# Performance work log

Measured on AMD Instinct MI355X. Metric: run time of the kernel, lower is better.

Reference implementation:

```python
import jax, jax.numpy as jnp
import numpy as np

B, H, W = 8, 160, 160
L = H * W  # 25600, matches nn.LayerNorm(25600)
QDIM = KDIM = MID = OUT = 256
HEADS = 8
HEAD_DIM = MID // HEADS  # 32
LN_EPS = 1e-5


def conv1x1(x, w, b):
    # x: [N,C,H,W], w: [O,C], b: [O] -> [N,O,H,W]
    return jnp.einsum('nchw,oc->nohw', x, w) + b[None, :, None, None]


def setup_inputs() -> dict:
    key = jax.random.key(0)
    ks = jax.random.split(key, 12)
    s = 0.02
    return {
        'query': jax.random.normal(ks[0], (B, QDIM, H, W), jnp.float32),
        'key': jax.random.normal(ks[1], (B, KDIM, H, W), jnp.float32),
        'Wq': jax.random.normal(ks[2], (MID, QDIM), jnp.float32) * s,
        'bq': jnp.zeros((MID,), jnp.float32),
        'Wk': jax.random.normal(ks[3], (MID, KDIM), jnp.float32) * s,
        'bk': jnp.zeros((MID,), jnp.float32),
        'Wv': jax.random.normal(ks[4], (MID, KDIM), jnp.float32) * s,
        'bv': jnp.zeros((MID,), jnp.float32),
        'Wo': jax.random.normal(ks[5], (OUT, MID), jnp.float32) * s,
        'bo': jnp.zeros((OUT,), jnp.float32),
        'gamma': jnp.ones((L,), jnp.float32),
        'beta': jnp.zeros((L,), jnp.float32),
    }


def reference(query, key, Wq, bq, Wk, bk, Wv, bv, Wo, bo, gamma, beta):
    # 1x1-conv projections, flatten spatial dims to L
    q = conv1x1(query, Wq, bq).reshape(B, HEADS, HEAD_DIM, L)
    k = conv1x1(key, Wk, bk).reshape(B, HEADS, HEAD_DIM, L)
    v = conv1x1(key, Wv, bv).reshape(B, HEADS, HEAD_DIM, L)
    # NOTE: faithful to the source, scores contract over L (spatial), giving
    # a [B, heads, head_dim, head_dim] channel-attention matrix.
    scores = jnp.einsum('nhdl,nhel->nhde', q, k) / (KDIM ** 0.5)
    attn = jax.nn.softmax(scores, axis=-1)  # dropout is identity at eval
    out = jnp.einsum('nhde,nhel->nhdl', attn, v).reshape(B, MID, L)
    # LayerNorm over the flattened spatial axis (size 25600)
    mu = jnp.mean(out, axis=-1, keepdims=True)
    var = jnp.var(out, axis=-1, keepdims=True)
    out = (out - mu) * jax.lax.rsqrt(var + LN_EPS) * gamma + beta
    out = out.reshape(B, MID, H, W)
    return conv1x1(out, Wo, bo)
```

## Files before the change

kernel.cpp:

```cpp
#include <hip/hip_runtime.h>
#include <hip/hip_bf16.h>
#include <stdint.h>

#define LROW 25600
#define NCH 256
#define LN_EPS 1e-5f

typedef float f32x4 __attribute__((ext_vector_type(4)));
typedef __bf16 bf16x8 __attribute__((ext_vector_type(8)));

__device__ __forceinline__ bf16x8 cvt8(f32x4 a, f32x4 b) {
  bf16x8 r;
  r[0] = (__bf16)a[0]; r[1] = (__bf16)a[1]; r[2] = (__bf16)a[2]; r[3] = (__bf16)a[3];
  r[4] = (__bf16)b[0]; r[5] = (__bf16)b[1]; r[6] = (__bf16)b[2]; r[7] = (__bf16)b[3];
  return r;
}

__device__ __forceinline__ void wg_bar() {
  asm volatile("s_waitcnt lgkmcnt(0)\n\ts_barrier" ::: "memory");
}

__global__ __launch_bounds__(1024, 4) void gram_k(
    const float* __restrict__ qg, const float* __restrict__ kg,
    float* __restrict__ Gd, float* __restrict__ Gkkd,
    float* __restrict__ sq, float* __restrict__ sk) {
  __shared__ __align__(16) __bf16 lA[256 * 32];
  __shared__ __align__(16) __bf16 lB[256 * 32];

  const int bid = blockIdx.x;
  const int x = bid & 7;
  int n = bid >> 3;
  int b = 0, s = 0;
  for (int bb = 0; bb < 8; ++bb) {
    const int gsl = (x - bb) & 7;
    const int gs = (21 * gsl + 7) >> 3, ge = (21 * gsl + 28) >> 3;
    const int ks = (11 * gsl + 7) >> 3, ke = (11 * gsl + 18) >> 3;
    const int cnt = (ge - gs) + (ke - ks);
    if (n < cnt) {
      b = bb;
      s = (n < ge - gs) ? (gs + n) : (21 + ks + (n - (ge - gs)));
      break;
    }
    n -= cnt;
  }

  const int mat = (s < 21) ? 0 : 1;
  const int idx = mat ? (s - 21) : s;
  const int parts = mat ? 11 : 21;
  const int c0 = (800 * idx) / parts, c1 = (800 * (idx + 1)) / parts;
  const int nc = c1 - c0;
  const int tid = threadIdx.x;
  const int w = tid >> 6, lane = tid & 63;
  const int wr = w >> 2, wc = w & 3;
  const int lr = lane & 15, g = lane >> 4;
  const float* Ag = (mat ? kg : qg) + (size_t)b * NCH * LROW;
  const float* Bg = kg + (size_t)b * NCH * LROW;

  const int rowS = tid >> 2, uS = tid & 3;
  const int uSw = uS ^ ((rowS >> 1) & 3);
  const size_t gOff = (size_t)rowS * LROW + uS * 8;
  __bf16* ldsA_dst = lA + rowS * 32 + uSw * 8;
  __bf16* ldsB_dst = lB + rowS * 32 + uSw * 8;

  const f32x4 zero = {0.f, 0.f, 0.f, 0.f};
  f32x4 acc[4][4];
#pragma unroll
  for (int i = 0; i < 4; ++i)
#pragma unroll
    for (int j = 0; j < 4; ++j) acc[i][j] = zero;

  float rsum = 0.f;

  auto LOADG = [&](int c, f32x4* d) {
    const float* pa = Ag + gOff + (size_t)c * 32;
    d[0] = *(const f32x4*)pa;
    d[1] = *(const f32x4*)(pa + 4);
    if (mat == 0) {
      const float* pb = Bg + gOff + (size_t)c * 32;
      d[2] = *(const f32x4*)pb;
      d[3] = *(const f32x4*)(pb + 4);
    }
  };

  auto PROCESS = [&](f32x4* d) {
#pragma unroll
    for (int e = 0; e < 4; ++e) rsum += d[0][e] + d[1][e];
    *(bf16x8*)ldsA_dst = cvt8(d[0], d[1]);
    if (mat == 0) *(bf16x8*)ldsB_dst = cvt8(d[2], d[3]);
    wg_bar();
    const __bf16* Bp = mat ? lA : lB;
    bf16x8 af[4];
#pragma unroll
    for (int i = 0; i < 4; ++i) {
      const int row = wr * 64 + i * 16 + lr;
      const int u = g ^ ((row >> 1) & 3);
      af[i] = *(const bf16x8*)(lA + row * 32 + u * 8);
    }
#pragma unroll
    for (int j = 0; j < 4; ++j) {
      const int row = wc * 64 + j * 16 + lr;
      const int u = g ^ ((row >> 1) & 3);
      bf16x8 bfj = *(const bf16x8*)(Bp + row * 32 + u * 8);
#pragma unroll
      for (int i = 0; i < 4; ++i)
        acc[i][j] = __builtin_amdgcn_mfma_f32_16x16x32_bf16(af[i], bfj, acc[i][j], 0, 0, 0);
    }
    wg_bar();
  };

  f32x4 bA[4], bB[4];
  LOADG(c0, bA);
  int cc = 0;
  for (; cc + 2 <= nc; cc += 2) {
    LOADG(c0 + cc + 1, bB);
    PROCESS(bA);
    if (cc + 2 < nc) LOADG(c0 + cc + 2, bA);
    PROCESS(bB);
  }
  if (cc < nc) PROCESS(bA);

  atomicAdd((mat ? sk : sq) + b * NCH + rowS, rsum);

  float* Gout = (mat ? Gkkd : Gd) + (size_t)b * 65536;
#pragma unroll
  for (int i = 0; i < 4; ++i)
#pragma unroll
    for (int j = 0; j < 4; ++j) {
      const int col = wc * 64 + j * 16 + lr;
      const int row0 = wr * 64 + i * 16 + g * 4;
#pragma unroll
      for (int r = 0; r < 4; ++r)
        atomicAdd(&Gout[(size_t)(row0 + r) * NCH + col], acc[i][j][r]);
    }
}

__global__ __launch_bounds__(256) void attn_k(
    const float* __restrict__ G, const float* __restrict__ sq,
    const float* __restrict__ sk,
    const float* __restrict__ Wq, const float* __restrict__ bq,
    const float* __restrict__ Wk, const float* __restrict__ bk,
    const float* __restrict__ Wv, const float* __restrict__ bv,
    float* __restrict__ M, float* __restrict__ cvec) {
  __shared__ float Wql[32][257];
  __shared__ float Wkl[32][257];
  __shared__ float QGl[32][257];
  __shared__ float Sl[32][33];
  __shared__ float Al[32][33];
  __shared__ float ul[32], wl[32];
  const int b = blockIdx.x >> 3, h = blockIdx.x & 7;
  const int t = threadIdx.x;
  const float* Gb = G + (size_t)b * 65536;

  for (int i = 0; i < 32; ++i) {
    int idx = i * 256 + t;
    int d = idx >> 8, c = idx & 255;
    Wql[d][c] = Wq[(h * 32 + d) * 256 + c];
    Wkl[d][c] = Wk[(h * 32 + d) * 256 + c];
  }
  __syncthreads();
  {
    float a[32];
#pragma unroll
    for (int d = 0; d < 32; ++d) a[d] = 0.f;
    for (int c = 0; c < 256; ++c) {
      float gv = Gb[c * 256 + t];
#pragma unroll
      for (int d = 0; d < 32; ++d) a[d] += Wql[d][c] * gv;
    }
    for (int d = 0; d < 32; ++d) QGl[d][t] = a[d];
  }
  if (t < 32) {
    float u = 0.f, wv = 0.f;
    for (int c = 0; c < 256; ++c) {
      u += Wql[t][c] * sq[b * 256 + c];
      wv += Wkl[t][c] * sk[b * 256 + c];
    }
    ul[t] = u; wl[t] = wv;
  }
  __syncthreads();
  for (int i = 0; i < 4; ++i) {
    int idx = i * 256 + t;
    int d = idx >> 5, e = idx & 31;
    float sv = 0.f;
    for (int c = 0; c < 256; ++c) sv += QGl[d][c] * Wkl[e][c];
    float bqd = bq[h * 32 + d], bke = bk[h * 32 + e];
    Sl[d][e] = (sv + ul[d] * bke + bqd * wl[e] + 25600.f * bqd * bke) * (1.f / 16.f);
  }
  __syncthreads();
  if (t < 32) {
    float m = -1e30f;
    for (int e = 0; e < 32; ++e) m = fmaxf(m, Sl[t][e]);
    float ssum = 0.f;
    for (int e = 0; e < 32; ++e) { float p = __expf(Sl[t][e] - m); Al[t][e] = p; ssum += p; }
    float is = 1.f / ssum;
    for (int e = 0; e < 32; ++e) Al[t][e] *= is;
  }
  __syncthreads();
  {
    float a[32];
#pragma unroll
    for (int d = 0; d < 32; ++d) a[d] = 0.f;
    for (int e = 0; e < 32; ++e) {
      float wv = Wv[(h * 32 + e) * 256 + t];
#pragma unroll
      for (int d = 0; d < 32; ++d) a[d] += Al[d][e] * wv;
    }
    for (int d = 0; d < 32; ++d) M[((size_t)b * 256 + h * 32 + d) * 256 + t] = a[d];
  }
  if (t < 32) {
    float cv = 0.f;
    for (int e = 0; e < 32; ++e) cv += Al[t][e] * bv[h * 32 + e];
    cvec[b * 256 + h * 32 + t] = cv;
  }
}

__global__ __launch_bounds__(256) void stats_k(
    const float* __restrict__ Gkk, const float* __restrict__ M,
    const float* __restrict__ sk, const float* __restrict__ cvec,
    float* __restrict__ mu, float* __restrict__ inv) {
  __shared__ float Ml[32][257];
  __shared__ float Ql[32][257];
  const int b = blockIdx.x >> 3, cb = blockIdx.x & 7;
  const int t = threadIdx.x;
  const float* Gk = Gkk + (size_t)b * 65536;
  for (int i = 0; i < 32; ++i) {
    int idx = i * 256 + t;
    Ml[idx >> 8][idx & 255] = M[((size_t)b * 256 + cb * 32 + (idx >> 8)) * 256 + (idx & 255)];
  }
  __syncthreads();
  {
    float a[32];
#pragma unroll
    for (int c = 0; c < 32; ++c) a[c] = 0.f;
    for (int cc = 0; cc < 256; ++cc) {
      float gv = Gk[cc * 256 + t];
#pragma unroll
      for (int c = 0; c < 32; ++c) a[c] += Ml[c][cc] * gv;
    }
    for (int c = 0; c < 32; ++c) Ql[c][t] = a[c];
  }
  __syncthreads();
  if (t < 32) {
    float qf = 0.f, msk = 0.f;
    for (int j = 0; j < 256; ++j) {
      qf += Ql[t][j] * Ml[t][j];
      msk += Ml[t][j] * sk[b * 256 + j];
    }
    int c = cb * 32 + t;
    float cv = cvec[b * 256 + c];
    float muv = msk * (1.f / 25600.f) + cv;
    float sum2 = qf + 2.f * cv * msk + 25600.f * cv * cv;
    float var = sum2 * (1.f / 25600.f) - muv * muv;
    mu[b * 256 + c] = muv;
    inv[b * 256 + c] = rsqrtf(var + LN_EPS);
  }
}

__global__ __launch_bounds__(256) void pmat_k(
    const float* __restrict__ M, const float* __restrict__ Wo,
    const float* __restrict__ inv, const float* __restrict__ cvec,
    const float* __restrict__ mu, __bf16* __restrict__ Pb,
    float* __restrict__ t1, float* __restrict__ wsum) {
  __shared__ float Wol[32][257];
  __shared__ float invl[256];
  const int b = blockIdx.x >> 3, ob = blockIdx.x & 7;
  const int t = threadIdx.x;
  invl[t] = inv[b * 256 + t];
  __syncthreads();
  for (int i = 0; i < 32; ++i) {
    int idx = i * 256 + t;
    int o = idx >> 8, c = idx & 255;
    Wol[o][c] = Wo[(ob * 32 + o) * 256 + c] * invl[c];
  }
  __syncthreads();
  {
    float a[32];
#pragma unroll
    for (int o = 0; o < 32; ++o) a[o] = 0.f;
    for (int c = 0; c < 256; ++c) {
      float m = M[((size_t)b * 256 + c) * 256 + t];
#pragma unroll
      for (int o = 0; o < 32; ++o) a[o] += Wol[o][c] * m;
    }
    for (int o = 0; o < 32; ++o)
      Pb[((size_t)b * 256 + ob * 32 + o) * 256 + t] = (__bf16)a[o];
  }
  if (t < 32) {
    float s1 = 0.f, s2 = 0.f;
    for (int c = 0; c < 256; ++c) {
      s1 += Wol[t][c] * (cvec[b * 256 + c] - mu[b * 256 + c]);
      s2 += Wo[(ob * 32 + t) * 256 + c];
    }
    t1[b * 256 + ob * 32 + t] = s1;
    wsum[b * 256 + ob * 32 + t] = s2;
  }
}

__global__ __launch_bounds__(512, 4) void outf_k(
    const float* __restrict__ key, const __bf16* __restrict__ Pb,
    const float* __restrict__ t1, const float* __restrict__ wsum,
    const float* __restrict__ bo, const float* __restrict__ gamma,
    const float* __restrict__ beta, float* __restrict__ out) {
  __shared__ __align__(16) __bf16 Bt[128 * 256];
  const int bid = blockIdx.x;
  const int b = bid / 200, lt = bid % 200, l0 = lt * 128;
  const int tid = threadIdx.x, w = tid >> 6, lane = tid & 63;
  const int wr = w >> 1, wc = w & 1;
  const int lr = lane & 15, g = lane >> 4;
  const float* Kb = key + (size_t)b * NCH * LROW;

  {
    const int c = tid & 255, seg = tid >> 8;
    const int uc = c >> 3, cb2 = (c & 7) * 2;
    const float* src = Kb + (size_t)c * LROW + l0 + seg * 64;
#pragma unroll
    for (int i = 0; i < 16; ++i) {
      f32x4 v = *(const f32x4*)(src + i * 4);
#pragma unroll
      for (int j = 0; j < 4; ++j) {
        const int l = seg * 64 + i * 4 + j;
        *(__bf16*)((char*)Bt + l * 512 + ((uc ^ (l & 7)) << 4) + cb2) = (__bf16)v[j];
      }
    }
  }
  __syncthreads();

  const f32x4 zero = {0.f, 0.f, 0.f, 0.f};
  f32x4 acc[4][4];
#pragma unroll
  for (int i = 0; i < 4; ++i)
#pragma unroll
    for (int j = 0; j < 4; ++j) acc[i][j] = zero;

  const __bf16* Pbase = Pb + (size_t)b * 65536;
#pragma unroll
  for (int ks = 0; ks < 8; ++ks) {
    bf16x8 af[4];
#pragma unroll
    for (int i = 0; i < 4; ++i) {
      const int row = wr * 64 + i * 16 + lr;
      af[i] = *(const bf16x8*)(Pbase + (size_t)row * 256 + ks * 32 + g * 8);
    }
#pragma unroll
    for (int j = 0; j < 4; ++j) {
      const int col = wc * 64 + j * 16 + lr;
      const int unit = ks * 4 + g;
      bf16x8 bfj = *(const bf16x8*)((const char*)Bt + col * 512 + ((unit ^ (col & 7)) << 4));
#pragma unroll
      for (int i = 0; i < 4; ++i)
        acc[i][j] = __builtin_amdgcn_mfma_f32_16x16x32_bf16(af[i], bfj, acc[i][j], 0, 0, 0);
    }
  }

  float t1r[4][4], wsr[4][4], bor[4][4];
#pragma unroll
  for (int i = 0; i < 4; ++i)
#pragma unroll
    for (int r = 0; r < 4; ++r) {
      const int row = wr * 64 + i * 16 + g * 4 + r;
      t1r[i][r] = t1[b * 256 + row];
      wsr[i][r] = wsum[b * 256 + row];
      bor[i][r] = bo[row];
    }
#pragma unroll
  for (int j = 0; j < 4; ++j) {
    const int colg = l0 + wc * 64 + j * 16 + lr;
    const float gm = gamma[colg];
    const float bt = beta[colg];
#pragma unroll
    for (int i = 0; i < 4; ++i) {
      const int row0 = wr * 64 + i * 16 + g * 4;
#pragma unroll
      for (int r = 0; r < 4; ++r) {
        const int row = row0 + r;
        float v = gm * (acc[i][j][r] + t1r[i][r]) + bt * wsr[i][r] + bor[i][r];
        out[((size_t)b * 256 + row) * LROW + colg] = v;
      }
    }
  }
}

extern "C" void kernel_launch(void* const* d_in, const int* in_sizes, int n_in,
                              void* d_out, int out_size, void* d_ws, size_t ws_size,
                              hipStream_t stream) {
  const float* query = (const float*)d_in[0];
  const float* key   = (const float*)d_in[1];
  const float* Wq = (const float*)d_in[2];
  const float* bq = (const float*)d_in[3];
  const float* Wk = (const float*)d_in[4];
  const float* bk = (const float*)d_in[5];
  const float* Wv = (const float*)d_in[6];
  const float* bv = (const float*)d_in[7];
  const float* Wo = (const float*)d_in[8];
  const float* bo = (const float*)d_in[9];
  const float* gamma = (const float*)d_in[10];
  const float* beta  = (const float*)d_in[11];
  float* out = (float*)d_out;

  float* ws = (float*)d_ws;
  float* G    = ws;
  float* Gkk  = G + 524288;
  float* sq   = Gkk + 524288;
  float* sk   = sq + 2048;
  float* M    = sk + 2048;
  float* cvec = M + 524288;
  float* mu   = cvec + 2048;
  float* inv  = mu + 2048;
  float* t1   = inv + 2048;
  float* wsum = t1 + 2048;
  __bf16* Pb  = (__bf16*)(wsum + 2048);

  hipMemsetAsync(d_ws, 0, (size_t)(524288 * 2 + 4096) * sizeof(float), stream);

  gram_k<<<256, 1024, 0, stream>>>(query, key, G, Gkk, sq, sk);
  attn_k<<<64, 256, 0, stream>>>(G, sq, sk, Wq, bq, Wk, bk, Wv, bv, M, cvec);
  stats_k<<<64, 256, 0, stream>>>(Gkk, M, sk, cvec, mu, inv);
  pmat_k<<<64, 256, 0, stream>>>(M, Wo, inv, cvec, mu, Pb, t1, wsum);
  outf_k<<<1600, 512, 0, stream>>>(key, Pb, t1, wsum, bo, gamma, beta, out);
}
```

Measured before the change: 707.1 us.

## Retile Gram kernel into 128x128 split-K tiles with double-buffered LDS

The Gram kernel now uses 256-thread blocks, each computing a 128x128 quadrant of G or Gkk over one of 12 K-slices, instead of 1024-thread blocks computing the full 256x256 matrix. It adds double-buffered LDS so there is one barrier per step rather than two, and the launch grows to 768 blocks. The aim is better occupancy and load/compute overlap. In exchange each input row is read several more times from memory (Gkk no longer reuses one load for both operands), which relies on cache reuse. The small attn/stats/pmat kernels drop their LDS staging of weights and read them directly from global in 8-wide chunks.

```diff
diff --git a/kernel.cpp b/kernel.cpp
--- a/kernel.cpp
+++ b/kernel.cpp
@@ -8,6 +8,7 @@
 
 typedef float f32x4 __attribute__((ext_vector_type(4)));
 typedef __bf16 bf16x8 __attribute__((ext_vector_type(8)));
+typedef __bf16 bf16x4 __attribute__((ext_vector_type(4)));
 
 __device__ __forceinline__ bf16x8 cvt8(f32x4 a, f32x4 b) {
   bf16x8 r;
@@ -20,47 +21,39 @@
   asm volatile("s_waitcnt lgkmcnt(0)\n\ts_barrier" ::: "memory");
 }
 
-__global__ __launch_bounds__(1024, 4) void gram_k(
+__global__ __launch_bounds__(256, 3) void gram_k(
     const float* __restrict__ qg, const float* __restrict__ kg,
     float* __restrict__ Gd, float* __restrict__ Gkkd,
     float* __restrict__ sq, float* __restrict__ sk) {
-  __shared__ __align__(16) __bf16 lA[256 * 32];
-  __shared__ __align__(16) __bf16 lB[256 * 32];
+  __shared__ __align__(16) __bf16 sA[2][128 * 32];
+  __shared__ __align__(16) __bf16 sB[2][128 * 32];
 
   const int bid = blockIdx.x;
   const int x = bid & 7;
-  int n = bid >> 3;
-  int b = 0, s = 0;
-  for (int bb = 0; bb < 8; ++bb) {
-    const int gsl = (x - bb) & 7;
-    const int gs = (21 * gsl + 7) >> 3, ge = (21 * gsl + 28) >> 3;
-    const int ks = (11 * gsl + 7) >> 3, ke = (11 * gsl + 18) >> 3;
-    const int cnt = (ge - gs) + (ke - ks);
-    if (n < cnt) {
-      b = bb;
-      s = (n < ge - gs) ? (gs + n) : (21 + ks + (n - (ge - gs)));
-      break;
-    }
-    n -= cnt;
-  }
-
-  const int mat = (s < 21) ? 0 : 1;
-  const int idx = mat ? (s - 21) : s;
-  const int parts = mat ? 11 : 21;
-  const int c0 = (800 * idx) / parts, c1 = (800 * (idx + 1)) / parts;
+  const int n = bid >> 3;
+  const int p = n % 12;
+  const int tile = n / 12;
+  const int gp = p * 8 + x;
+  const int b = gp / 12, ks = gp % 12;
+  const int mat = tile >> 2;
+  const int ri = (tile >> 1) & 1, ci = tile & 1;
+  const int c0 = (800 * ks) / 12, c1 = (800 * (ks + 1)) / 12;
   const int nc = c1 - c0;
+
   const int tid = threadIdx.x;
   const int w = tid >> 6, lane = tid & 63;
-  const int wr = w >> 2, wc = w & 3;
+  const int wr = w >> 1, wc = w & 1;
   const int lr = lane & 15, g = lane >> 4;
-  const float* Ag = (mat ? kg : qg) + (size_t)b * NCH * LROW;
-  const float* Bg = kg + (size_t)b * NCH * LROW;
-
-  const int rowS = tid >> 2, uS = tid & 3;
-  const int uSw = uS ^ ((rowS >> 1) & 3);
-  const size_t gOff = (size_t)rowS * LROW + uS * 8;
-  __bf16* ldsA_dst = lA + rowS * 32 + uSw * 8;
-  __bf16* ldsB_dst = lB + rowS * 32 + uSw * 8;
+
+  const float* Abase = (mat ? kg : qg) + (size_t)b * NCH * LROW + (size_t)(ri * 128) * LROW;
+  const float* Bbase = kg + (size_t)b * NCH * LROW + (size_t)(ci * 128) * LROW;
+
+  const int rowS = tid >> 1, hf = tid & 1;
+  const float* Ap = Abase + (size_t)rowS * LROW + hf * 16 + (size_t)c0 * 32;
+  const float* Bp = Bbase + (size_t)rowS * LROW + hf * 16 + (size_t)c0 * 32;
+  const int swS = (rowS >> 1) & 3;
+  const int dA0 = rowS * 32 + ((2 * hf) ^ swS) * 8;
+  const int dA1 = rowS * 32 + ((2 * hf + 1) ^ swS) * 8;
 
   const f32x4 zero = {0.f, 0.f, 0.f, 0.f};
   f32x4 acc[4][4];
@@ -70,58 +63,59 @@
     for (int j = 0; j < 4; ++j) acc[i][j] = zero;
 
   float rsum = 0.f;
+  f32x4 rA[8], rB[8];
 
   auto LOADG = [&](int c, f32x4* d) {
-    const float* pa = Ag + gOff + (size_t)c * 32;
-    d[0] = *(const f32x4*)pa;
-    d[1] = *(const f32x4*)(pa + 4);
-    if (mat == 0) {
-      const float* pb = Bg + gOff + (size_t)c * 32;
-      d[2] = *(const f32x4*)pb;
-      d[3] = *(const f32x4*)(pb + 4);
-    }
+    const float* pa = Ap + (size_t)c * 32;
+#pragma unroll
+    for (int i = 0; i < 4; ++i) d[i] = *(const f32x4*)(pa + i * 4);
+    const float* pb = Bp + (size_t)c * 32;
+#pragma unroll
+    for (int i = 0; i < 4; ++i) d[4 + i] = *(const f32x4*)(pb + i * 4);
   };
-
-  auto PROCESS = [&](f32x4* d) {
-#pragma unroll
-    for (int e = 0; e < 4; ++e) rsum += d[0][e] + d[1][e];
-    *(bf16x8*)ldsA_dst = cvt8(d[0], d[1]);
-    if (mat == 0) *(bf16x8*)ldsB_dst = cvt8(d[2], d[3]);
-    wg_bar();
-    const __bf16* Bp = mat ? lA : lB;
+  auto WRITE = [&](f32x4* d, int buf) {
+#pragma unroll
+    for (int e = 0; e < 4; ++e)
+      rsum += d[0][e] + d[1][e] + d[2][e] + d[3][e];
+    *(bf16x8*)(&sA[buf][dA0]) = cvt8(d[0], d[1]);
+    *(bf16x8*)(&sA[buf][dA1]) = cvt8(d[2], d[3]);
+    *(bf16x8*)(&sB[buf][dA0]) = cvt8(d[4], d[5]);
+    *(bf16x8*)(&sB[buf][dA1]) = cvt8(d[6], d[7]);
+  };
+  auto COMPUTE = [&](int buf) {
     bf16x8 af[4];
 #pragma unroll
     for (int i = 0; i < 4; ++i) {
       const int row = wr * 64 + i * 16 + lr;
-      const int u = g ^ ((row >> 1) & 3);
-      af[i] = *(const bf16x8*)(lA + row * 32 + u * 8);
+      af[i] = *(const bf16x8*)(&sA[buf][row * 32 + ((g ^ ((row >> 1) & 3)) * 8)]);
     }
 #pragma unroll
     for (int j = 0; j < 4; ++j) {
       const int row = wc * 64 + j * 16 + lr;
-      const int u = g ^ ((row >> 1) & 3);
-      bf16x8 bfj = *(const bf16x8*)(Bp + row * 32 + u * 8);
+      bf16x8 bfj = *(const bf16x8*)(&sB[buf][row * 32 + ((g ^ ((row >> 1) & 3)) * 8)]);
 #pragma unroll
       for (int i = 0; i < 4; ++i)
         acc[i][j] = __builtin_amdgcn_mfma_f32_16x16x32_bf16(af[i], bfj, acc[i][j], 0, 0, 0);
     }
-    wg_bar();
   };
 
-  f32x4 bA[4], bB[4];
-  LOADG(c0, bA);
+  LOADG(0, rA);
   int cc = 0;
   for (; cc + 2 <= nc; cc += 2) {
-    LOADG(c0 + cc + 1, bB);
-    PROCESS(bA);
-    if (cc + 2 < nc) LOADG(c0 + cc + 2, bA);
-    PROCESS(bB);
-  }
-  if (cc < nc) PROCESS(bA);
-
-  atomicAdd((mat ? sk : sq) + b * NCH + rowS, rsum);
-
-  float* Gout = (mat ? Gkkd : Gd) + (size_t)b * 65536;
+    WRITE(rA, 0);
+    if (cc + 1 < nc) LOADG(cc + 1, rB);
+    wg_bar();
+    COMPUTE(0);
+    WRITE(rB, 1);
+    if (cc + 2 < nc) LOADG(cc + 2, rA);
+    wg_bar();
+    COMPUTE(1);
+  }
+  if (cc < nc) { WRITE(rA, 0); wg_bar(); COMPUTE(0); }
+
+  if (ci == 0) atomicAdd((mat ? sk : sq) + b * NCH + ri * 128 + rowS, rsum);
+
+  float* Gout = (mat ? Gkkd : Gd) + (size_t)b * 65536 + (size_t)(ri * 128) * 256 + ci * 128;
 #pragma unroll
   for (int i = 0; i < 4; ++i)
 #pragma unroll
@@ -130,7 +124,7 @@
       const int row0 = wr * 64 + i * 16 + g * 4;
 #pragma unroll
       for (int r = 0; r < 4; ++r)
-        atomicAdd(&Gout[(size_t)(row0 + r) * NCH + col], acc[i][j][r]);
+        atomicAdd(&Gout[(size_t)(row0 + r) * 256 + col], acc[i][j][r]);
     }
 }
 
@@ -141,7 +135,6 @@
     const float* __restrict__ Wk, const float* __restrict__ bk,
     const float* __restrict__ Wv, const float* __restrict__ bv,
     float* __restrict__ M, float* __restrict__ cvec) {
-  __shared__ float Wql[32][257];
   __shared__ float Wkl[32][257];
   __shared__ float QGl[32][257];
   __shared__ float Sl[32][33];
@@ -150,34 +143,40 @@
   const int b = blockIdx.x >> 3, h = blockIdx.x & 7;
   const int t = threadIdx.x;
   const float* Gb = G + (size_t)b * 65536;
+  const float* WqB = Wq + h * 32 * 256;
+  const float* WkB = Wk + h * 32 * 256;
 
   for (int i = 0; i < 32; ++i) {
     int idx = i * 256 + t;
-    int d = idx >> 8, c = idx & 255;
-    Wql[d][c] = Wq[(h * 32 + d) * 256 + c];
-    Wkl[d][c] = Wk[(h * 32 + d) * 256 + c];
-  }
-  __syncthreads();
+    Wkl[idx >> 8][idx & 255] = WkB[idx];
+  }
+  __syncthreads();
+
   {
     float a[32];
 #pragma unroll
     for (int d = 0; d < 32; ++d) a[d] = 0.f;
-    for (int c = 0; c < 256; ++c) {
-      float gv = Gb[c * 256 + t];
-#pragma unroll
-      for (int d = 0; d < 32; ++d) a[d] += Wql[d][c] * gv;
+    for (int cb = 0; cb < 256; cb += 8) {
+      float gv[8];
+#pragma unroll
+      for (int j = 0; j < 8; ++j) gv[j] = Gb[(cb + j) * 256 + t];
+#pragma unroll
+      for (int d = 0; d < 32; ++d)
+#pragma unroll
+        for (int j = 0; j < 8; ++j) a[d] += WqB[d * 256 + cb + j] * gv[j];
     }
     for (int d = 0; d < 32; ++d) QGl[d][t] = a[d];
   }
   if (t < 32) {
     float u = 0.f, wv = 0.f;
     for (int c = 0; c < 256; ++c) {
-      u += Wql[t][c] * sq[b * 256 + c];
-      wv += Wkl[t][c] * sk[b * 256 + c];
+      u += WqB[t * 256 + c] * sq[b * 256 + c];
+      wv += WkB[t * 256 + c] * sk[b * 256 + c];
     }
     ul[t] = u; wl[t] = wv;
   }
   __syncthreads();
+
   for (int i = 0; i < 4; ++i) {
     int idx = i * 256 + t;
     int d = idx >> 5, e = idx & 31;
@@ -191,7 +190,7 @@
     float m = -1e30f;
     for (int e = 0; e < 32; ++e) m = fmaxf(m, Sl[t][e]);
     float ssum = 0.f;
-    for (int e = 0; e < 32; ++e) { float p = __expf(Sl[t][e] - m); Al[t][e] = p; ssum += p; }
+    for (int e = 0; e < 32; ++e) { float pp = __expf(Sl[t][e] - m); Al[t][e] = pp; ssum += pp; }
     float is = 1.f / ssum;
     for (int e = 0; e < 32; ++e) Al[t][e] *= is;
   }
@@ -218,24 +217,24 @@
     const float* __restrict__ Gkk, const float* __restrict__ M,
     const float* __restrict__ sk, const float* __restrict__ cvec,
     float* __restrict__ mu, float* __restrict__ inv) {
-  __shared__ float Ml[32][257];
   __shared__ float Ql[32][257];
   const int b = blockIdx.x >> 3, cb = blockIdx.x & 7;
   const int t = threadIdx.x;
   const float* Gk = Gkk + (size_t)b * 65536;
-  for (int i = 0; i < 32; ++i) {
-    int idx = i * 256 + t;
-    Ml[idx >> 8][idx & 255] = M[((size_t)b * 256 + cb * 32 + (idx >> 8)) * 256 + (idx & 255)];
-  }
-  __syncthreads();
+  const float* Mrow = M + ((size_t)b * 256 + cb * 32) * 256;
+
   {
     float a[32];
 #pragma unroll
     for (int c = 0; c < 32; ++c) a[c] = 0.f;
-    for (int cc = 0; cc < 256; ++cc) {
-      float gv = Gk[cc * 256 + t];
-#pragma unroll
-      for (int c = 0; c < 32; ++c) a[c] += Ml[c][cc] * gv;
+    for (int ccb = 0; ccb < 256; ccb += 8) {
+      float gk[8];
+#pragma unroll
+      for (int j = 0; j < 8; ++j) gk[j] = Gk[(ccb + j) * 256 + t];
+#pragma unroll
+      for (int c = 0; c < 32; ++c)
+#pragma unroll
+        for (int j = 0; j < 8; ++j) a[c] += Mrow[c * 256 + ccb + j] * gk[j];
     }
     for (int c = 0; c < 32; ++c) Ql[c][t] = a[c];
   }
@@ -243,8 +242,9 @@
   if (t < 32) {
     float qf = 0.f, msk = 0.f;
     for (int j = 0; j < 256; ++j) {
-      qf += Ql[t][j] * Ml[t][j];
-      msk += Ml[t][j] * sk[b * 256 + j];
+      float mv = Mrow[t * 256 + j];
+      qf += Ql[t][j] * mv;
+      msk += mv * sk[b * 256 + j];
     }
     int c = cb * 32 + t;
     float cv = cvec[b * 256 + c];
@@ -261,26 +261,22 @@
     const float* __restrict__ inv, const float* __restrict__ cvec,
     const float* __restrict__ mu, __bf16* __restrict__ Pb,
     float* __restrict__ t1, float* __restrict__ wsum) {
-  __shared__ float Wol[32][257];
-  __shared__ float invl[256];
   const int b = blockIdx.x >> 3, ob = blockIdx.x & 7;
   const int t = threadIdx.x;
-  invl[t] = inv[b * 256 + t];
-  __syncthreads();
-  for (int i = 0; i < 32; ++i) {
-    int idx = i * 256 + t;
-    int o = idx >> 8, c = idx & 255;
-    Wol[o][c] = Wo[(ob * 32 + o) * 256 + c] * invl[c];
-  }
-  __syncthreads();
+  const float* WoB = Wo + ob * 32 * 256;
   {
     float a[32];
 #pragma unroll
     for (int o = 0; o < 32; ++o) a[o] = 0.f;
-    for (int c = 0; c < 256; ++c) {
-      float m = M[((size_t)b * 256 + c) * 256 + t];
-#pragma unroll
-      for (int o = 0; o < 32; ++o) a[o] += Wol[o][c] * m;
+    for (int cbk = 0; cbk < 256; cbk += 8) {
+      float ig[8];
+#pragma unroll
+      for (int j = 0; j < 8; ++j)
+        ig[j] = inv[b * 256 + cbk + j] * M[((size_t)b * 256 + cbk + j) * 256 + t];
+#pragma unroll
+      for (int o = 0; o < 32; ++o)
+#pragma unroll
+        for (int j = 0; j < 8; ++j) a[o] += WoB[o * 256 + cbk + j] * ig[j];
     }
     for (int o = 0; o < 32; ++o)
       Pb[((size_t)b * 256 + ob * 32 + o) * 256 + t] = (__bf16)a[o];
@@ -288,8 +284,9 @@
   if (t < 32) {
     float s1 = 0.f, s2 = 0.f;
     for (int c = 0; c < 256; ++c) {
-      s1 += Wol[t][c] * (cvec[b * 256 + c] - mu[b * 256 + c]);
-      s2 += Wo[(ob * 32 + t) * 256 + c];
+      float wo = WoB[t * 256 + c];
+      s1 += wo * inv[b * 256 + c] * (cvec[b * 256 + c] - mu[b * 256 + c]);
+      s2 += wo;
     }
     t1[b * 256 + ob * 32 + t] = s1;
     wsum[b * 256 + ob * 32 + t] = s2;
@@ -412,7 +409,7 @@
 
   hipMemsetAsync(d_ws, 0, (size_t)(524288 * 2 + 4096) * sizeof(float), stream);
 
-  gram_k<<<256, 1024, 0, stream>>>(query, key, G, Gkk, sq, sk);
+  gram_k<<<768, 256, 0, stream>>>(query, key, G, Gkk, sq, sk);
   attn_k<<<64, 256, 0, stream>>>(G, sq, sk, Wq, bq, Wk, bk, Wv, bv, M, cvec);
   stats_k<<<64, 256, 0, stream>>>(Gkk, M, sk, cvec, mu, inv);
   pmat_k<<<64, 256, 0, stream>>>(M, Wo, inv, cvec, mu, Pb, t1, wsum);
```

Measured after the change: 1.100 ms. 1.56x slower.

## Fuse Gram computations per block, use split-K partials, and halve outf tile

Applied to the files above, without the earlier changes.

The Gram kernel now computes Q·Kᵀ and K·Kᵀ in the same block, sharing the K tile, with double-buffered LDS and an even split of 32 chunks per batch. It writes per-split partials to workspace that a new reduce kernel sums, replacing contended float atomics when the workspace is large enough. The output kernel also moves to 64-column tiles with more blocks and higher occupancy, using a wider swizzle. This trades a 128 MB partial-buffer write and read, plus an extra launch, for removing the atomics and the duplicated K loads.

```diff
diff --git a/kernel.cpp b/kernel.cpp
--- a/kernel.cpp
+++ b/kernel.cpp
@@ -20,118 +20,143 @@
   asm volatile("s_waitcnt lgkmcnt(0)\n\ts_barrier" ::: "memory");
 }
 
+template <int FULL>
 __global__ __launch_bounds__(1024, 4) void gram_k(
     const float* __restrict__ qg, const float* __restrict__ kg,
-    float* __restrict__ Gd, float* __restrict__ Gkkd,
+    float* __restrict__ P0,
+    float* __restrict__ P1,
     float* __restrict__ sq, float* __restrict__ sk) {
-  __shared__ __align__(16) __bf16 lA[256 * 32];
-  __shared__ __align__(16) __bf16 lB[256 * 32];
+  __shared__ __align__(16) __bf16 lq[2][256 * 32];
+  __shared__ __align__(16) __bf16 lk[2][256 * 32];
 
   const int bid = blockIdx.x;
-  const int x = bid & 7;
-  int n = bid >> 3;
-  int b = 0, s = 0;
-  for (int bb = 0; bb < 8; ++bb) {
-    const int gsl = (x - bb) & 7;
-    const int gs = (21 * gsl + 7) >> 3, ge = (21 * gsl + 28) >> 3;
-    const int ks = (11 * gsl + 7) >> 3, ke = (11 * gsl + 18) >> 3;
-    const int cnt = (ge - gs) + (ke - ks);
-    if (n < cnt) {
-      b = bb;
-      s = (n < ge - gs) ? (gs + n) : (21 + ks + (n - (ge - gs)));
-      break;
-    }
-    n -= cnt;
-  }
-
-  const int mat = (s < 21) ? 0 : 1;
-  const int idx = mat ? (s - 21) : s;
-  const int parts = mat ? 11 : 21;
-  const int c0 = (800 * idx) / parts, c1 = (800 * (idx + 1)) / parts;
-  const int nc = c1 - c0;
+  const int b = bid >> 5, s = bid & 31;
+  const int c0 = s * 25;
+  const int nc = 25;
+
   const int tid = threadIdx.x;
   const int w = tid >> 6, lane = tid & 63;
   const int wr = w >> 2, wc = w & 3;
   const int lr = lane & 15, g = lane >> 4;
-  const float* Ag = (mat ? kg : qg) + (size_t)b * NCH * LROW;
-  const float* Bg = kg + (size_t)b * NCH * LROW;
-
-  const int rowS = tid >> 2, uS = tid & 3;
-  const int uSw = uS ^ ((rowS >> 1) & 3);
-  const size_t gOff = (size_t)rowS * LROW + uS * 8;
-  __bf16* ldsA_dst = lA + rowS * 32 + uSw * 8;
-  __bf16* ldsB_dst = lB + rowS * 32 + uSw * 8;
+
+  const int rS = tid >> 2, q4 = tid & 3;
+  const float* gq = qg + (size_t)b * NCH * LROW + (size_t)rS * LROW + q4 * 8;
+  const float* gk = kg + (size_t)b * NCH * LROW + (size_t)rS * LROW + q4 * 8;
+  const int offS = rS * 32 + ((q4 ^ (rS & 3)) * 8);
 
   const f32x4 zero = {0.f, 0.f, 0.f, 0.f};
-  f32x4 acc[4][4];
+  f32x4 accG[4][4], accK[4][4];
 #pragma unroll
   for (int i = 0; i < 4; ++i)
 #pragma unroll
-    for (int j = 0; j < 4; ++j) acc[i][j] = zero;
-
-  float rsum = 0.f;
+    for (int j = 0; j < 4; ++j) { accG[i][j] = zero; accK[i][j] = zero; }
+
+  float rsq = 0.f, rsk = 0.f;
+  f32x4 bA[4], bB[4];
 
   auto LOADG = [&](int c, f32x4* d) {
-    const float* pa = Ag + gOff + (size_t)c * 32;
-    d[0] = *(const f32x4*)pa;
-    d[1] = *(const f32x4*)(pa + 4);
-    if (mat == 0) {
-      const float* pb = Bg + gOff + (size_t)c * 32;
-      d[2] = *(const f32x4*)pb;
-      d[3] = *(const f32x4*)(pb + 4);
-    }
+    const float* pq = gq + (size_t)c * 32;
+    d[0] = *(const f32x4*)pq;
+    d[1] = *(const f32x4*)(pq + 4);
+    const float* pk = gk + (size_t)c * 32;
+    d[2] = *(const f32x4*)pk;
+    d[3] = *(const f32x4*)(pk + 4);
   };
-
-  auto PROCESS = [&](f32x4* d) {
-#pragma unroll
-    for (int e = 0; e < 4; ++e) rsum += d[0][e] + d[1][e];
-    *(bf16x8*)ldsA_dst = cvt8(d[0], d[1]);
-    if (mat == 0) *(bf16x8*)ldsB_dst = cvt8(d[2], d[3]);
-    wg_bar();
-    const __bf16* Bp = mat ? lA : lB;
-    bf16x8 af[4];
+  auto WRITE = [&](f32x4* d, int buf) {
+#pragma unroll
+    for (int e = 0; e < 4; ++e) {
+      rsq += d[0][e] + d[1][e];
+      rsk += d[2][e] + d[3][e];
+    }
+    *(bf16x8*)(&lq[buf][offS]) = cvt8(d[0], d[1]);
+    *(bf16x8*)(&lk[buf][offS]) = cvt8(d[2], d[3]);
+  };
+  auto COMPUTE = [&](int buf) {
+    bf16x8 aq[4], ak[4];
 #pragma unroll
     for (int i = 0; i < 4; ++i) {
       const int row = wr * 64 + i * 16 + lr;
-      const int u = g ^ ((row >> 1) & 3);
-      af[i] = *(const bf16x8*)(lA + row * 32 + u * 8);
+      const int off = row * 32 + ((g ^ (row & 3)) * 8);
+      aq[i] = *(const bf16x8*)(&lq[buf][off]);
+      ak[i] = *(const bf16x8*)(&lk[buf][off]);
     }
 #pragma unroll
     for (int j = 0; j < 4; ++j) {
       const int row = wc * 64 + j * 16 + lr;
-      const int u = g ^ ((row >> 1) & 3);
-      bf16x8 bfj = *(const bf16x8*)(Bp + row * 32 + u * 8);
-#pragma unroll
-      for (int i = 0; i < 4; ++i)
-        acc[i][j] = __builtin_amdgcn_mfma_f32_16x16x32_bf16(af[i], bfj, acc[i][j], 0, 0, 0);
-    }
-    wg_bar();
+      const int off = row * 32 + ((g ^ (row & 3)) * 8);
+      bf16x8 bk = *(const bf16x8*)(&lk[buf][off]);
+#pragma unroll
+      for (int i = 0; i < 4; ++i) {
+        accG[i][j] = __builtin_amdgcn_mfma_f32_16x16x32_bf16(aq[i], bk, accG[i][j], 0, 0, 0);
+        accK[i][j] = __builtin_amdgcn_mfma_f32_16x16x32_bf16(ak[i], bk, accK[i][j], 0, 0, 0);
+      }
+    }
   };
 
-  f32x4 bA[4], bB[4];
-  LOADG(c0, bA);
+  LOADG(c0 + 0, bA);
+  LOADG(c0 + 1, bB);
   int cc = 0;
   for (; cc + 2 <= nc; cc += 2) {
-    LOADG(c0 + cc + 1, bB);
-    PROCESS(bA);
+    WRITE(bA, 0);
+    wg_bar();
     if (cc + 2 < nc) LOADG(c0 + cc + 2, bA);
-    PROCESS(bB);
-  }
-  if (cc < nc) PROCESS(bA);
-
-  atomicAdd((mat ? sk : sq) + b * NCH + rowS, rsum);
-
-  float* Gout = (mat ? Gkkd : Gd) + (size_t)b * 65536;
-#pragma unroll
-  for (int i = 0; i < 4; ++i)
-#pragma unroll
-    for (int j = 0; j < 4; ++j) {
-      const int col = wc * 64 + j * 16 + lr;
-      const int row0 = wr * 64 + i * 16 + g * 4;
-#pragma unroll
-      for (int r = 0; r < 4; ++r)
-        atomicAdd(&Gout[(size_t)(row0 + r) * NCH + col], acc[i][j][r]);
-    }
+    COMPUTE(0);
+    WRITE(bB, 1);
+    wg_bar();
+    if (cc + 3 < nc) LOADG(c0 + cc + 3, bB);
+    COMPUTE(1);
+  }
+  if (cc < nc) { WRITE(bA, 0); wg_bar(); COMPUTE(0); }
+
+  rsq += __shfl_xor(rsq, 1); rsq += __shfl_xor(rsq, 2);
+  rsk += __shfl_xor(rsk, 1); rsk += __shfl_xor(rsk, 2);
+  if (q4 == 0) {
+    atomicAdd(sq + b * NCH + rS, rsq);
+    atomicAdd(sk + b * NCH + rS, rsk);
+  }
+
+  if (FULL) {
+    float* Gout = P0 + (size_t)(b * 32 + s) * 131072;
+#pragma unroll
+    for (int i = 0; i < 4; ++i)
+#pragma unroll
+      for (int j = 0; j < 4; ++j) {
+        const int col = wc * 64 + j * 16 + lr;
+        const int row0 = wr * 64 + i * 16 + g * 4;
+#pragma unroll
+        for (int r = 0; r < 4; ++r) {
+          Gout[(size_t)(row0 + r) * 256 + col] = accG[i][j][r];
+          Gout[65536 + (size_t)(row0 + r) * 256 + col] = accK[i][j][r];
+        }
+      }
+  } else {
+    float* Gd = P0 + (size_t)b * 65536;
+    float* Gkkd = P1 + (size_t)b * 65536;
+#pragma unroll
+    for (int i = 0; i < 4; ++i)
+#pragma unroll
+      for (int j = 0; j < 4; ++j) {
+        const int col = wc * 64 + j * 16 + lr;
+        const int row0 = wr * 64 + i * 16 + g * 4;
+#pragma unroll
+        for (int r = 0; r < 4; ++r) {
+          atomicAdd(&Gd[(size_t)(row0 + r) * 256 + col], accG[i][j][r]);
+          atomicAdd(&Gkkd[(size_t)(row0 + r) * 256 + col], accK[i][j][r]);
+        }
+      }
+  }
+}
+
+__global__ __launch_bounds__(256) void reduce_k(
+    const float* __restrict__ Pp, float* __restrict__ G, float* __restrict__ Gkk) {
+  const int f = (blockIdx.x * 256 + threadIdx.x) * 4;
+  const int b = f >> 17, r = f & 131071;
+  f32x4 a = {0.f, 0.f, 0.f, 0.f};
+#pragma unroll
+  for (int si = 0; si < 32; ++si)
+    a += *(const f32x4*)(Pp + (size_t)(b * 32 + si) * 131072 + r);
+  if (r < 65536) *(f32x4*)(G + (size_t)b * 65536 + r) = a;
+  else *(f32x4*)(Gkk + (size_t)b * 65536 + (r - 65536)) = a;
 }
 
 __global__ __launch_bounds__(256) void attn_k(
@@ -191,7 +216,7 @@
     float m = -1e30f;
     for (int e = 0; e < 32; ++e) m = fmaxf(m, Sl[t][e]);
     float ssum = 0.f;
-    for (int e = 0; e < 32; ++e) { float p = __expf(Sl[t][e] - m); Al[t][e] = p; ssum += p; }
+    for (int e = 0; e < 32; ++e) { float pp = __expf(Sl[t][e] - m); Al[t][e] = pp; ssum += pp; }
     float is = 1.f / ssum;
     for (int e = 0; e < 32; ++e) Al[t][e] *= is;
   }
@@ -296,41 +321,41 @@
   }
 }
 
-__global__ __launch_bounds__(512, 4) void outf_k(
+__global__ __launch_bounds__(512, 8) void outf_k(
     const float* __restrict__ key, const __bf16* __restrict__ Pb,
     const float* __restrict__ t1, const float* __restrict__ wsum,
     const float* __restrict__ bo, const float* __restrict__ gamma,
     const float* __restrict__ beta, float* __restrict__ out) {
-  __shared__ __align__(16) __bf16 Bt[128 * 256];
+  __shared__ __align__(16) __bf16 Bt[64 * 256];
   const int bid = blockIdx.x;
-  const int b = bid / 200, lt = bid % 200, l0 = lt * 128;
+  const int b = bid / 400, lt = bid % 400, l0 = lt * 64;
   const int tid = threadIdx.x, w = tid >> 6, lane = tid & 63;
   const int wr = w >> 1, wc = w & 1;
   const int lr = lane & 15, g = lane >> 4;
   const float* Kb = key + (size_t)b * NCH * LROW;
 
   {
-    const int c = tid & 255, seg = tid >> 8;
-    const int uc = c >> 3, cb2 = (c & 7) * 2;
-    const float* src = Kb + (size_t)c * LROW + l0 + seg * 64;
-#pragma unroll
-    for (int i = 0; i < 16; ++i) {
-      f32x4 v = *(const f32x4*)(src + i * 4);
+    const int c = tid >> 1, u0 = tid & 1;
+    const int cu = c >> 3, ce2 = (c & 7) * 2;
+    const float* src = Kb + (size_t)c * LROW + l0 + u0 * 32;
+#pragma unroll
+    for (int x = 0; x < 8; ++x) {
+      f32x4 v = *(const f32x4*)(src + x * 4);
 #pragma unroll
       for (int j = 0; j < 4; ++j) {
-        const int l = seg * 64 + i * 4 + j;
-        *(__bf16*)((char*)Bt + l * 512 + ((uc ^ (l & 7)) << 4) + cb2) = (__bf16)v[j];
+        const int l = u0 * 32 + x * 4 + j;
+        *(__bf16*)((char*)Bt + l * 512 + ((cu ^ (l & 31)) << 4) + ce2) = (__bf16)v[j];
       }
     }
   }
   __syncthreads();
 
   const f32x4 zero = {0.f, 0.f, 0.f, 0.f};
-  f32x4 acc[4][4];
+  f32x4 acc[4][2];
 #pragma unroll
   for (int i = 0; i < 4; ++i)
 #pragma unroll
-    for (int j = 0; j < 4; ++j) acc[i][j] = zero;
+    for (int j = 0; j < 2; ++j) acc[i][j] = zero;
 
   const __bf16* Pbase = Pb + (size_t)b * 65536;
 #pragma unroll
@@ -342,10 +367,10 @@
       af[i] = *(const bf16x8*)(Pbase + (size_t)row * 256 + ks * 32 + g * 8);
     }
 #pragma unroll
-    for (int j = 0; j < 4; ++j) {
-      const int col = wc * 64 + j * 16 + lr;
-      const int unit = ks * 4 + g;
-      bf16x8 bfj = *(const bf16x8*)((const char*)Bt + col * 512 + ((unit ^ (col & 7)) << 4));
+    for (int j = 0; j < 2; ++j) {
+      const int col = wc * 32 + j * 16 + lr;
+      bf16x8 bfj = *(const bf16x8*)((const char*)Bt + col * 512 +
+                                    (((ks * 4 + g) ^ (col & 31)) << 4));
 #pragma unroll
       for (int i = 0; i < 4; ++i)
         acc[i][j] = __builtin_amdgcn_mfma_f32_16x16x32_bf16(af[i], bfj, acc[i][j], 0, 0, 0);
@@ -363,8 +388,8 @@
       bor[i][r] = bo[row];
     }
 #pragma unroll
-  for (int j = 0; j < 4; ++j) {
-    const int colg = l0 + wc * 64 + j * 16 + lr;
+  for (int j = 0; j < 2; ++j) {
+    const int colg = l0 + wc * 32 + j * 16 + lr;
     const float gm = gamma[colg];
     const float bt = beta[colg];
 #pragma unroll
@@ -409,12 +434,19 @@
   float* t1   = inv + 2048;
   float* wsum = t1 + 2048;
   __bf16* Pb  = (__bf16*)(wsum + 2048);
-
-  hipMemsetAsync(d_ws, 0, (size_t)(524288 * 2 + 4096) * sizeof(float), stream);
-
-  gram_k<<<256, 1024, 0, stream>>>(query, key, G, Gkk, sq, sk);
+  float* Pp = ws + 1847296;
+  const size_t need = (size_t)(1847296 + 33554432) * 4;
+
+  if (ws_size >= need) {
+    hipMemsetAsync(sq, 0, 4096 * sizeof(float), stream);
+    gram_k<1><<<256, 1024, 0, stream>>>(query, key, Pp, nullptr, sq, sk);
+    reduce_k<<<1024, 256, 0, stream>>>(Pp, G, Gkk);
+  } else {
+    hipMemsetAsync(d_ws, 0, (size_t)1052672 * sizeof(float), stream);
+    gram_k<0><<<256, 1024, 0, stream>>>(query, key, G, Gkk, sq, sk);
+  }
   attn_k<<<64, 256, 0, stream>>>(G, sq, sk, Wq, bq, Wk, bk, Wv, bv, M, cvec);
   stats_k<<<64, 256, 0, stream>>>(Gkk, M, sk, cvec, mu, inv);
   pmat_k<<<64, 256, 0, stream>>>(M, Wo, inv, cvec, mu, Pb, t1, wsum);
-  outf_k<<<1600, 512, 0, stream>>>(key, Pb, t1, wsum, bo, gamma, beta, out);
-}
+  outf_k<<<3200, 512, 0, stream>>>(key, Pb, t1, wsum, bo, gamma, beta, out);
+}
```

New measurement: 1.675 ms. +136.9%, slower.
